# Kernel optimization log

Hardware: AMD Instinct MI355X
Metric: run time of the kernel (lower is better)

## Reference

```python
import jax, jax.numpy as jnp
import numpy as np

N_NODES, N_EDGES = 50000, 800000
IN_X, OUT_X = 32, 64
IN_EN, OUT_EN = 32, 64
HIDDEN = [64, 128, 32]  # build_mlp hidden sizes


def _mlp_params(key, dims):
    ps = []
    for i, (a, b) in enumerate(zip(dims[:-1], dims[1:])):
        k1, k2, key = jax.random.split(key, 3)
        s = 1.0 / np.sqrt(a)
        ps.append(jax.random.uniform(k1, (a, b), jnp.float32, -s, s))
        ps.append(jax.random.uniform(k2, (b,), jnp.float32, -s, s))
    return ps


def _mlp_apply(h, params):
    n_layers = len(params) // 2
    for i in range(n_layers):
        W, b = params[2 * i], params[2 * i + 1]
        h = h @ W + b
        if i < n_layers - 1:
            h = jax.nn.relu(h)
    return h


def setup_inputs() -> dict:
    key = jax.random.key(0)
    kx, ken, ks, kd, kt, kp, k_ten, k_pen = jax.random.split(key, 8)
    inp = {
        "x": jax.random.normal(kx, (N_NODES, IN_X), jnp.float32),
        "en": jax.random.normal(ken, (N_NODES, IN_EN), jnp.float32),
        "src": jax.random.randint(ks, (N_EDGES,), 0, N_NODES),
        "dst": jax.random.randint(kd, (N_EDGES,), 0, N_NODES),
    }
    # linear layers theta/phi for x
    kt1, kt2 = jax.random.split(kt)
    kp1, kp2 = jax.random.split(kp)
    s = 1.0 / np.sqrt(IN_X)
    inp["theta_W"] = jax.random.uniform(kt1, (IN_X, OUT_X), jnp.float32, -s, s)
    inp["theta_b"] = jax.random.uniform(kt2, (OUT_X,), jnp.float32, -s, s)
    inp["phi_W"] = jax.random.uniform(kp1, (IN_X, OUT_X), jnp.float32, -s, s)
    inp["phi_b"] = jax.random.uniform(kp2, (OUT_X,), jnp.float32, -s, s)
    # MLPs theta_en / phi_en: in_en -> 64 -> 128 -> 32 -> out_en
    dims = [IN_EN] + HIDDEN + [OUT_EN]
    for name, p in zip(
        ["ten_W0", "ten_b0", "ten_W1", "ten_b1", "ten_W2", "ten_b2", "ten_W3", "ten_b3"],
        _mlp_params(k_ten, dims)):
        inp[name] = p
    for name, p in zip(
        ["pen_W0", "pen_b0", "pen_W1", "pen_b1", "pen_W2", "pen_b2", "pen_W3", "pen_b3"],
        _mlp_params(k_pen, dims)):
        inp[name] = p
    return inp


def reference(x, en, src, dst,
              theta_W, theta_b, phi_W, phi_b,
              ten_W0, ten_b0, ten_W1, ten_b1, ten_W2, ten_b2, ten_W3, ten_b3,
              pen_W0, pen_b0, pen_W1, pen_b1, pen_W2, pen_b2, pen_W3, pen_b3):
    n = x.shape[0]
    ten = [ten_W0, ten_b0, ten_W1, ten_b1, ten_W2, ten_b2, ten_W3, ten_b3]
    pen = [pen_W0, pen_b0, pen_W1, pen_b1, pen_W2, pen_b2, pen_W3, pen_b3]

    # --- message: per-edge features ---
    dx = x[dst] - x[src]                       # [E, in_x]
    edge_x = dx @ theta_W + theta_b + (x @ phi_W + phi_b)[src]   # [E, out_x]
    den = en[dst] - en[src]                    # [E, in_en]
    edge_en = _mlp_apply(den, ten) + _mlp_apply(en, pen)[src]    # [E, out_en]

    # --- aggregate: max over incoming edge_x, mean over incoming edge_en ---
    deg = jax.ops.segment_sum(jnp.ones((src.shape[0],), x.dtype), dst, num_segments=n)
    has_in = (deg > 0)[:, None]
    x_new = jax.ops.segment_max(edge_x, dst, num_segments=n)
    x_new = jnp.where(has_in, x_new, 0.0)      # DGL zero-fills empty nodes
    en_sum = jax.ops.segment_sum(edge_en, dst, num_segments=n)
    en_new = en_sum / jnp.maximum(deg, 1.0)[:, None]

    # knn_graph rebuild is a library call (excluded from the kernel target);
    # return the updated node features carried by the new graph.
    return jnp.concatenate([x_new, en_new], axis=-1)  # [N, out_x + out_en]
```

## Files before the change

### kernel.cpp

```cpp
#include <hip/hip_runtime.h>

#define N_NODES 50000
#define N_EDGES 800000

typedef __attribute__((ext_vector_type(8))) short short8v;
typedef __attribute__((ext_vector_type(4))) float f32x4;

__device__ __forceinline__ ushort bf16hi(float v) {
  return (ushort)(__float_as_uint(v) >> 16);
}

__device__ __forceinline__ void split8(const float v[8], short8v& hh, short8v& ll) {
#pragma unroll
  for (int j = 0; j < 8; ++j) {
    unsigned uv = __float_as_uint(v[j]);
    hh[j] = (short)(uv >> 16);
    float hf = __uint_as_float(uv & 0xFFFF0000u);
    ll[j] = (short)(__float_as_uint(v[j] - hf) >> 16);
  }
}

#define C1_X 196
#define C1_CNT 3125
#define C1_PACK 120

constexpr int XK_THT = 0;
constexpr int XK_PHT = 2048;
constexpr int XK_THB = 4096;
constexpr int XK_PHB = 4160;
constexpr int XK_SZ  = 4224;

__global__ void __launch_bounds__(256) combo1_kernel(
    const float* __restrict__ x,
    const float* __restrict__ thW, const float* __restrict__ thB,
    const float* __restrict__ phW, const float* __restrict__ phB,
    float* __restrict__ out, float* __restrict__ gp,
    const int* __restrict__ dst, int* __restrict__ counts,
    const float* __restrict__ tW1, const float* __restrict__ tW2,
    const float* __restrict__ tW0, const float* __restrict__ pW0,
    const float* __restrict__ pW1, const float* __restrict__ pW2,
    const float* __restrict__ pW3, ushort* __restrict__ wp) {
  const int b = blockIdx.x;
  const int tid = threadIdx.x;
  if (b < C1_X) {
    __shared__ __align__(16) float sm[XK_SZ];
    for (int t = tid; t < 2048; t += 256) {
      int j = t >> 5, k = t & 31;
      sm[XK_THT + t] = thW[k * 64 + j];
      sm[XK_PHT + t] = phW[k * 64 + j];
    }
    for (int t = tid; t < 64; t += 256) {
      sm[XK_THB + t] = thB[t];
      sm[XK_PHB + t] = phB[t];
    }
    __syncthreads();
    int n = b * 256 + tid;
    if (n >= N_NODES) return;

    float xv[32];
    {
      const float4* p = (const float4*)(x + (long)n * 32);
#pragma unroll
      for (int q = 0; q < 8; ++q) {
        float4 v = p[q];
        xv[q * 4 + 0] = v.x; xv[q * 4 + 1] = v.y;
        xv[q * 4 + 2] = v.z; xv[q * 4 + 3] = v.w;
      }
    }
    float* ao = out + (long)n * 128;
    float* go = gp + (long)n * 128;
    for (int j = 0; j < 64; ++j) {
      float dth = 0.f, dph = 0.f;
#pragma unroll
      for (int k = 0; k < 32; ++k) {
        dth += xv[k] * sm[XK_THT + j * 32 + k];
        dph += xv[k] * sm[XK_PHT + j * 32 + k];
      }
      ao[j] = sm[XK_THB + j] + dth;
      go[j] = sm[XK_PHB + j] + dph - dth;
    }
  } else if (b < C1_X + C1_CNT) {
    int e = (b - C1_X) * 256 + tid;
    if (e < N_EDGES) atomicAdd(&counts[dst[e]], 1);
  } else {
    int t = (b - C1_X - C1_CNT) * 256 + tid;
    if (t >= 30720) return;
    float v;
    int hi_off, lo_off;
    if (t < 8192) {
      int fi = t >> 9, lane = (t >> 3) & 63, j = t & 7;
      int r = fi >> 1, f = fi & 1;
      int row = r * 16 + (lane & 15);
      int sig = 32 * f + 16 * (j >> 2) + 4 * ((lane >> 4) & 3) + (j & 3);
      v = tW1[sig * 128 + row];
      hi_off = t; lo_off = 8192 + t;
    } else if (t < 12288) {
      int t2 = t - 8192;
      int fi = t2 >> 9, lane = (t2 >> 3) & 63, j = t2 & 7;
      int tt = fi >> 2, f2 = fi & 3;
      int cc = tt * 16 + (lane & 15);
      int qq = (lane >> 4) & 3;
      int k2 = f2 * 32 + (j >> 2) * 16 + qq * 4 + (j & 3);
      v = tW2[k2 * 32 + cc];
      hi_off = 16384 + t2; lo_off = 20480 + t2;
    } else if (t < 14336) {
      int t3 = t - 12288;
      int fi = t3 >> 9, lane = (t3 >> 3) & 63, j = t3 & 7;
      int row = fi * 16 + (lane & 15);
      int k = (lane >> 4) * 8 + j;
      v = tW0[k * 64 + row];
      hi_off = 24576 + t3; lo_off = 26624 + t3;
    } else if (t < 16384) {
      int t4 = t - 14336;
      int fi = t4 >> 9, lane = (t4 >> 3) & 63, j = t4 & 7;
      int row = fi * 16 + (lane & 15);
      int k = (lane >> 4) * 8 + j;
      v = pW0[k * 64 + row];
      hi_off = 28672 + t4; lo_off = 30720 + t4;
    } else if (t < 24576) {
      int t5 = t - 16384;
      int fi = t5 >> 9, lane = (t5 >> 3) & 63, j = t5 & 7;
      int r = fi >> 1, f = fi & 1;
      int row = r * 16 + (lane & 15);
      int sig = 32 * f + 16 * (j >> 2) + 4 * ((lane >> 4) & 3) + (j & 3);
      v = pW1[sig * 128 + row];
      hi_off = 32768 + t5; lo_off = 40960 + t5;
    } else if (t < 28672) {
      int t6 = t - 24576;
      int fi = t6 >> 9, lane = (t6 >> 3) & 63, j = t6 & 7;
      int tt = fi >> 2, f2 = fi & 3;
      int cc = tt * 16 + (lane & 15);
      int qq = (lane >> 4) & 3;
      int k2 = f2 * 32 + (j >> 2) * 16 + qq * 4 + (j & 3);
      v = pW2[k2 * 32 + cc];
      hi_off = 49152 + t6; lo_off = 53248 + t6;
    } else {
      int t7 = t - 28672;
      int fi = t7 >> 9, lane = (t7 >> 3) & 63, j = t7 & 7;
      int row = fi * 16 + (lane & 15);
      int sig = 16 * (j >> 2) + 4 * ((lane >> 4) & 3) + (j & 3);
      v = pW3[sig * 64 + row];
      hi_off = 57344 + t7; lo_off = 59392 + t7;
    }
    ushort h = bf16hi(v);
    float hf = __uint_as_float((unsigned)h << 16);
    ushort l = bf16hi(v - hf);
    wp[hi_off] = h;
    wp[lo_off] = l;
  }
}

#define SCAN_NB ((N_NODES + 1023) / 1024)

__global__ void __launch_bounds__(1024) scan1_kernel(
    const int* __restrict__ counts, int* __restrict__ offsets,
    int* __restrict__ bsum) {
  __shared__ int wsum[16];
  int t = threadIdx.x, b = blockIdx.x;
  int idx = b * 1024 + t;
  int c = (idx < N_NODES) ? counts[idx] : 0;
  int lane = t & 63, w = t >> 6;
  int v = c;
#pragma unroll
  for (int off = 1; off < 64; off <<= 1) {
    int tt = __shfl_up(v, off);
    if (lane >= off) v += tt;
  }
  if (lane == 63) wsum[w] = v;
  __syncthreads();
  int wpre = 0;
#pragma unroll
  for (int i = 0; i < 16; ++i) {
    int tt = wsum[i];
    if (i < w) wpre += tt;
  }
  int incl = v + wpre;
  if (idx < N_NODES) offsets[idx] = incl - c;
  if (t == 1023) bsum[b] = incl;
}

__global__ void __launch_bounds__(1024) scan2_kernel(
    const int* __restrict__ bsum, int* __restrict__ offsets,
    int* __restrict__ counts) {
  __shared__ int sb[SCAN_NB];
  int t = threadIdx.x, b = blockIdx.x;
  if (t < SCAN_NB) sb[t] = bsum[t];
  __syncthreads();
  int bpre = 0;
#pragma unroll
  for (int i = 0; i < SCAN_NB; ++i) {
    int tt = sb[i];
    if (i < b) bpre += tt;
  }
  int idx = b * 1024 + t;
  if (idx < N_NODES) {
    int v = offsets[idx] + bpre;
    offsets[idx] = v;
    counts[idx] = v;
  }
  if (b == 0 && t == 0) offsets[N_NODES] = N_EDGES;
}

#define C2_EN 391
#define C2_SC 1563

__global__ void __launch_bounds__(512) combo2_kernel(
    const float* __restrict__ en, const ushort* __restrict__ wp,
    const float* __restrict__ pb0, const float* __restrict__ pb1,
    const float* __restrict__ pb2, const float* __restrict__ pb3,
    float* __restrict__ gp,
    const int* __restrict__ src, const int* __restrict__ dst,
    int* __restrict__ cursor, int2* __restrict__ csr) {
  const int b = blockIdx.x;
  const int tid = threadIdx.x;
  if (b < C2_EN) {
    __shared__ __align__(16) ushort lds[32768];
    {
      const uint4* s4 = (const uint4*)(wp + 28672);
      uint4* d4 = (uint4*)lds;
      for (int i = tid; i < 4096; i += 512) d4[i] = s4[i];
    }
    __syncthreads();
    const int lane = tid & 63, q = lane >> 4, c = lane & 15, wv = tid >> 6;
    const int n = (b * 8 + wv) * 16 + c;
    const bool valid = n < N_NODES;

    float env[8];
#pragma unroll
    for (int j = 0; j < 8; ++j) env[j] = 0.f;
    if (valid) {
      const float4* p = (const float4*)(en + (long)n * 32 + q * 8);
      float4 e0 = p[0], e1 = p[1];
      env[0] = e0.x; env[1] = e0.y; env[2] = e0.z; env[3] = e0.w;
      env[4] = e1.x; env[5] = e1.y; env[6] = e1.z; env[7] = e1.w;
    }
    short8v beh, bel;
    split8(env, beh, bel);

    const short8v* PW0H = (const short8v*)(lds);
    const short8v* PW0L = (const short8v*)(lds + 2048);
    const short8v* NW1H = (const short8v*)(lds + 4096);
    const short8v* NW1L = (const short8v*)(lds + 12288);
    const short8v* NW2H = (const short8v*)(lds + 20480);
    const short8v* NW2L = (const short8v*)(lds + 24576);
    const short8v* NW3H = (const short8v*)(lds + 28672);
    const short8v* NW3L = (const short8v*)(lds + 30720);

    float h0v[4][4];
#pragma unroll
    for (int t = 0; t < 4; ++t) {
      f32x4 a = *(const f32x4*)(pb0 + t * 16 + q * 4);
      short8v ah = PW0H[t * 64 + lane], al = PW0L[t * 64 + lane];
      a = __builtin_amdgcn_mfma_f32_16x16x32_bf16(ah, beh, a, 0, 0, 0);
      a = __builtin_amdgcn_mfma_f32_16x16x32_bf16(al, beh, a, 0, 0, 0);
      a = __builtin_amdgcn_mfma_f32_16x16x32_bf16(ah, bel, a, 0, 0, 0);
#pragma unroll
      for (int g = 0; g < 4; ++g) h0v[t][g] = fmaxf(a[g], 0.f);
    }

    short8v b1h[2], b1l[2];
#pragma unroll
    for (int f = 0; f < 2; ++f) {
      float tmp[8];
#pragma unroll
      for (int j = 0; j < 8; ++j) tmp[j] = h0v[2 * f + (j >> 2)][j & 3];
      split8(tmp, b1h[f], b1l[f]);
    }

    float h1v[8][4];
#pragma unroll
    for (int r = 0; r < 8; ++r) {
      f32x4 a = *(const f32x4*)(pb1 + r * 16 + q * 4);
#pragma unroll
      for (int f = 0; f < 2; ++f) {
        short8v ah = NW1H[(r * 2 + f) * 64 + lane];
        short8v al = NW1L[(r * 2 + f) * 64 + lane];
        a = __builtin_amdgcn_mfma_f32_16x16x32_bf16(ah, b1h[f], a, 0, 0, 0);
        a = __builtin_amdgcn_mfma_f32_16x16x32_bf16(al, b1h[f], a, 0, 0, 0);
        a = __builtin_amdgcn_mfma_f32_16x16x32_bf16(ah, b1l[f], a, 0, 0, 0);
      }
#pragma unroll
      for (int g = 0; g < 4; ++g) h1v[r][g] = fmaxf(a[g], 0.f);
    }

    short8v b2h[4], b2l[4];
#pragma unroll
    for (int f2 = 0; f2 < 4; ++f2) {
      float tmp[8];
#pragma unroll
      for (int j = 0; j < 8; ++j) tmp[j] = h1v[2 * f2 + (j >> 2)][j & 3];
      split8(tmp, b2h[f2], b2l[f2]);
    }

    float h2v[2][4];
#pragma unroll
    for (int tt = 0; tt < 2; ++tt) {
      f32x4 a = *(const f32x4*)(pb2 + tt * 16 + q * 4);
#pragma unroll
      for (int f2 = 0; f2 < 4; ++f2) {
        short8v ah = NW2H[(tt * 4 + f2) * 64 + lane];
        short8v al = NW2L[(tt * 4 + f2) * 64 + lane];
        a = __builtin_amdgcn_mfma_f32_16x16x32_bf16(ah, b2h[f2], a, 0, 0, 0);
        a = __builtin_amdgcn_mfma_f32_16x16x32_bf16(al, b2h[f2], a, 0, 0, 0);
        a = __builtin_amdgcn_mfma_f32_16x16x32_bf16(ah, b2l[f2], a, 0, 0, 0);
      }
#pragma unroll
      for (int g = 0; g < 4; ++g) h2v[tt][g] = fmaxf(a[g], 0.f);
    }

    short8v b3h, b3l;
    {
      float tmp[8];
#pragma unroll
      for (int j = 0; j < 8; ++j) tmp[j] = h2v[j >> 2][j & 3];
      split8(tmp, b3h, b3l);
    }

#pragma unroll
    for (int t = 0; t < 4; ++t) {
      f32x4 a = *(const f32x4*)(pb3 + t * 16 + q * 4);
      short8v ah = NW3H[t * 64 + lane], al = NW3L[t * 64 + lane];
      a = __builtin_amdgcn_mfma_f32_16x16x32_bf16(ah, b3h, a, 0, 0, 0);
      a = __builtin_amdgcn_mfma_f32_16x16x32_bf16(al, b3h, a, 0, 0, 0);
      a = __builtin_amdgcn_mfma_f32_16x16x32_bf16(ah, b3l, a, 0, 0, 0);
      if (valid) *(f32x4*)(gp + (long)n * 128 + 64 + t * 16 + q * 4) = a;
    }
  } else {
    int e = (b - C2_EN) * 512 + tid;
    if (e >= N_EDGES) return;
    int d = dst[e];
    int slot = atomicAdd(&cursor[d], 1);
    csr[slot] = make_int2(src[e], d);
  }
}

__global__ void __launch_bounds__(1024) mlp_edge_kernel(
    const float* __restrict__ en,
    const int2* __restrict__ csr,
    const float* __restrict__ b0g, const float* __restrict__ b1g,
    const float* __restrict__ b2g,
    const ushort* __restrict__ wp,
    float* __restrict__ h2sum) {
  __shared__ __align__(16) ushort lds[28672];
  {
    const uint4* s4 = (const uint4*)wp;
    uint4* d4 = (uint4*)lds;
    for (int i = threadIdx.x; i < 3584; i += 1024) d4[i] = s4[i];
  }
  __syncthreads();

  const int orig = blockIdx.x;
  const int xcd = orig & 7, loc = orig >> 3;
  const int blk = (xcd < 5) ? xcd * 391 + loc
                            : 5 * 391 + (xcd - 5) * 390 + loc;

  const int lane = threadIdx.x & 63;
  const int q = lane >> 4, c = lane & 15;
  const int wv = threadIdx.x >> 6;
  const int e = (blk * 16 + wv) * 16 + c;
  const int2 pr = csr[e];
  const int s = pr.x, d = pr.y;

  const short8v* W1HI = (const short8v*)(lds);
  const short8v* W1LO = (const short8v*)(lds + 8192);
  const short8v* W2HI = (const short8v*)(lds + 16384);
  const short8v* W2LO = (const short8v*)(lds + 20480);
  const short8v* W0H  = (const short8v*)(lds + 24576);
  const short8v* W0L  = (const short8v*)(lds + 26624);

  short8v dh, dl;
  {
    const float4* pd = (const float4*)(en + (long)d * 32 + q * 8);
    const float4* ps = (const float4*)(en + (long)s * 32 + q * 8);
    float4 a0 = pd[0], a1 = pd[1], b0 = ps[0], b1 = ps[1];
    float v[8];
    v[0] = a0.x - b0.x; v[1] = a0.y - b0.y;
    v[2] = a0.z - b0.z; v[3] = a0.w - b0.w;
    v[4] = a1.x - b1.x; v[5] = a1.y - b1.y;
    v[6] = a1.z - b1.z; v[7] = a1.w - b1.w;
    split8(v, dh, dl);
  }

  float h0v[4][4];
#pragma unroll
  for (int t = 0; t < 4; ++t) {
    f32x4 a = *(const f32x4*)(b0g + t * 16 + q * 4);
    short8v ah = W0H[t * 64 + lane], al = W0L[t * 64 + lane];
    a = __builtin_amdgcn_mfma_f32_16x16x32_bf16(ah, dh, a, 0, 0, 0);
    a = __builtin_amdgcn_mfma_f32_16x16x32_bf16(al, dh, a, 0, 0, 0);
    a = __builtin_amdgcn_mfma_f32_16x16x32_bf16(ah, dl, a, 0, 0, 0);
#pragma unroll
    for (int g = 0; g < 4; ++g) h0v[t][g] = fmaxf(a[g], 0.f);
  }

  short8v b1h[2], b1l[2];
#pragma unroll
  for (int f = 0; f < 2; ++f) {
    float tmp[8];
#pragma unroll
    for (int j = 0; j < 8; ++j) tmp[j] = h0v[2 * f + (j >> 2)][j & 3];
    split8(tmp, b1h[f], b1l[f]);
  }

  float h1v[8][4];
#pragma unroll
  for (int r = 0; r < 8; ++r) {
    f32x4 a = *(const f32x4*)(b1g + r * 16 + q * 4);
#pragma unroll
    for (int f = 0; f < 2; ++f) {
      short8v ah = W1HI[(r * 2 + f) * 64 + lane];
      short8v al = W1LO[(r * 2 + f) * 64 + lane];
      a = __builtin_amdgcn_mfma_f32_16x16x32_bf16(ah, b1h[f], a, 0, 0, 0);
      a = __builtin_amdgcn_mfma_f32_16x16x32_bf16(al, b1h[f], a, 0, 0, 0);
      a = __builtin_amdgcn_mfma_f32_16x16x32_bf16(ah, b1l[f], a, 0, 0, 0);
    }
#pragma unroll
    for (int g = 0; g < 4; ++g) h1v[r][g] = fmaxf(a[g], 0.f);
  }

  short8v b2h[4], b2l[4];
#pragma unroll
  for (int f2 = 0; f2 < 4; ++f2) {
    float tmp[8];
#pragma unroll
    for (int j = 0; j < 8; ++j) tmp[j] = h1v[2 * f2 + (j >> 2)][j & 3];
    split8(tmp, b2h[f2], b2l[f2]);
  }

  f32x4 a20 = *(const f32x4*)(b2g + q * 4);
  f32x4 a21 = *(const f32x4*)(b2g + 16 + q * 4);
#pragma unroll
  for (int f2 = 0; f2 < 4; ++f2) {
    short8v ah = W2HI[f2 * 64 + lane];
    short8v al = W2LO[f2 * 64 + lane];
    a20 = __builtin_amdgcn_mfma_f32_16x16x32_bf16(ah, b2h[f2], a20, 0, 0, 0);
    a20 = __builtin_amdgcn_mfma_f32_16x16x32_bf16(al, b2h[f2], a20, 0, 0, 0);
    a20 = __builtin_amdgcn_mfma_f32_16x16x32_bf16(ah, b2l[f2], a20, 0, 0, 0);
    short8v ah1 = W2HI[(4 + f2) * 64 + lane];
    short8v al1 = W2LO[(4 + f2) * 64 + lane];
    a21 = __builtin_amdgcn_mfma_f32_16x16x32_bf16(ah1, b2h[f2], a21, 0, 0, 0);
    a21 = __builtin_amdgcn_mfma_f32_16x16x32_bf16(al1, b2h[f2], a21, 0, 0, 0);
    a21 = __builtin_amdgcn_mfma_f32_16x16x32_bf16(ah1, b2l[f2], a21, 0, 0, 0);
  }
  float h2v[8];
#pragma unroll
  for (int g = 0; g < 4; ++g) {
    h2v[g] = fmaxf(a20[g], 0.f);
    h2v[4 + g] = fmaxf(a21[g], 0.f);
  }

  int dp = __shfl_up(d, 1, 16);
  bool head = (c == 0) || (dp != d);
  int seg = head ? c : 0;
#pragma unroll
  for (int off = 1; off < 16; off <<= 1) {
    int t = __shfl_up(seg, off, 16);
    if (c >= off) seg = max(seg, t);
  }
#pragma unroll
  for (int off = 1; off < 16; off <<= 1) {
    bool take = (c - off) >= seg;
#pragma unroll
    for (int k = 0; k < 8; ++k) {
      float t = __shfl_up(h2v[k], off, 16);
      if (take) h2v[k] += t;
    }
  }
  int dn = __shfl_down(d, 1, 16);
  bool tail = (c == 15) || (dn != d);
  if (tail) {
    float* hs = h2sum + (long)d * 32 + q * 4;
#pragma unroll
    for (int g = 0; g < 4; ++g) atomicAdd(&hs[g], h2v[g]);
#pragma unroll
    for (int g = 0; g < 4; ++g) atomicAdd(&hs[16 + g], h2v[4 + g]);
  }
}

__global__ void __launch_bounds__(256) gather_kernel(
    const int2* __restrict__ csr, const int* __restrict__ offsets,
    const float* __restrict__ gp, const float* __restrict__ h2sum,
    const float* __restrict__ tW3, const float* __restrict__ tb3,
    float* __restrict__ out) {
  __shared__ float sW3[2048 + 64];
  for (int t = threadIdx.x; t < 2048; t += 256) sW3[t] = tW3[t];
  for (int t = threadIdx.x; t < 64; t += 256) sW3[2048 + t] = tb3[t];
  __syncthreads();
  int n = blockIdx.x * 8 + (threadIdx.x >> 5);
  int l = threadIdx.x & 31;
  int half = l >> 4, j4 = l & 15;
  int off = half * 64 + j4 * 4;
  int o0 = offsets[n], o1 = offsets[n + 1];
  int deg = o1 - o0;

  const float NEG = -3.402823466e38f;
  float4 mx = make_float4(NEG, NEG, NEG, NEG);
  float4 sm4 = make_float4(0.f, 0.f, 0.f, 0.f);
  for (int t = o0; t < o1; ++t) {
    int s = csr[t].x;
    float4 v = *(const float4*)(gp + (long)s * 128 + off);
    mx.x = fmaxf(mx.x, v.x); mx.y = fmaxf(mx.y, v.y);
    mx.z = fmaxf(mx.z, v.z); mx.w = fmaxf(mx.w, v.w);
    sm4.x += v.x; sm4.y += v.y; sm4.z += v.z; sm4.w += v.w;
  }

  float4 r;
  if (half == 0) {
    float4 a = *(const float4*)(out + (long)n * 128 + off);
    bool has = deg > 0;
    r.x = has ? a.x + mx.x : 0.f;
    r.y = has ? a.y + mx.y : 0.f;
    r.z = has ? a.z + mx.z : 0.f;
    r.w = has ? a.w + mx.w : 0.f;
  } else {
    int jj = j4 * 4;
    float w30 = 0.f, w31 = 0.f, w32 = 0.f, w33 = 0.f;
    const float* h2r = h2sum + (long)n * 32;
#pragma unroll
    for (int k = 0; k < 32; ++k) {
      float h = h2r[k];
      const float* wrow = &sW3[k * 64 + jj];
      w30 += h * wrow[0]; w31 += h * wrow[1];
      w32 += h * wrow[2]; w33 += h * wrow[3];
    }
    float dg = (float)deg;
    float inv = 1.f / fmaxf(dg, 1.f);
    r.x = (sm4.x + w30 + dg * sW3[2048 + jj + 0]) * inv;
    r.y = (sm4.y + w31 + dg * sW3[2048 + jj + 1]) * inv;
    r.z = (sm4.z + w32 + dg * sW3[2048 + jj + 2]) * inv;
    r.w = (sm4.w + w33 + dg * sW3[2048 + jj + 3]) * inv;
  }
  *(float4*)(out + (long)n * 128 + off) = r;
}

extern "C" void kernel_launch(void* const* d_in, const int* in_sizes, int n_in,
                              void* d_out, int out_size, void* d_ws,
                              size_t ws_size, hipStream_t stream) {
  const float* x   = (const float*)d_in[0];
  const float* en  = (const float*)d_in[1];
  const int* src   = (const int*)d_in[2];
  const int* dst   = (const int*)d_in[3];
  const float* thW = (const float*)d_in[4];
  const float* thB = (const float*)d_in[5];
  const float* phW = (const float*)d_in[6];
  const float* phB = (const float*)d_in[7];
  const float* tW0 = (const float*)d_in[8];
  const float* tb0 = (const float*)d_in[9];
  const float* tW1 = (const float*)d_in[10];
  const float* tb1 = (const float*)d_in[11];
  const float* tW2 = (const float*)d_in[12];
  const float* tb2 = (const float*)d_in[13];
  const float* tW3 = (const float*)d_in[14];
  const float* tb3 = (const float*)d_in[15];
  const float* pW0 = (const float*)d_in[16];
  const float* pb0 = (const float*)d_in[17];
  const float* pW1 = (const float*)d_in[18];
  const float* pb1 = (const float*)d_in[19];
  const float* pW2 = (const float*)d_in[20];
  const float* pb2 = (const float*)d_in[21];
  const float* pW3 = (const float*)d_in[22];
  const float* pb3 = (const float*)d_in[23];

  float* out = (float*)d_out;
  float* ws  = (float*)d_ws;
  float* gp     = ws;
  float* h2sum  = ws + (long)N_NODES * 128;
  float* wpf    = ws + (long)N_NODES * 160;
  ushort* wp    = (ushort*)wpf;
  int* iw       = (int*)(wpf + 30720);
  int2* csr     = (int2*)iw;
  int* counts   = iw + 2 * N_EDGES;
  int* offsets  = counts + N_NODES;
  int* bsum     = offsets + N_NODES + 1;

  hipMemsetAsync(counts, 0, N_NODES * sizeof(int), stream);
  hipMemsetAsync(h2sum, 0, (size_t)N_NODES * 32 * sizeof(float), stream);
  combo1_kernel<<<C1_X + C1_CNT + C1_PACK, 256, 0, stream>>>(
      x, thW, thB, phW, phB, out, gp, dst, counts,
      tW1, tW2, tW0, pW0, pW1, pW2, pW3, wp);
  scan1_kernel<<<SCAN_NB, 1024, 0, stream>>>(counts, offsets, bsum);
  scan2_kernel<<<SCAN_NB, 1024, 0, stream>>>(bsum, offsets, counts);
  combo2_kernel<<<C2_EN + C2_SC, 512, 0, stream>>>(
      en, wp, pb0, pb1, pb2, pb3, gp, src, dst, counts, csr);
  mlp_edge_kernel<<<3125, 1024, 0, stream>>>(
      en, csr, tb0, tb1, tb2, wp, h2sum);
  gather_kernel<<<N_NODES / 8, 256, 0, stream>>>(
      csr, offsets, gp, h2sum, tW3, tb3, out);
}
```

Baseline: 315.2 us.

## Fuse node gather into edge MLP kernel and split out a light finalize pass

```diff
diff --git a/kernel.cpp b/kernel.cpp
--- a/kernel.cpp
+++ b/kernel.cpp
@@ -334,23 +334,64 @@
   }
 }
 
-__global__ void __launch_bounds__(1024) mlp_edge_kernel(
+#define EG_NB 4689
+
+__global__ void __launch_bounds__(1024) edge_gather_kernel(
     const float* __restrict__ en,
     const int2* __restrict__ csr,
     const float* __restrict__ b0g, const float* __restrict__ b1g,
     const float* __restrict__ b2g,
     const ushort* __restrict__ wp,
-    float* __restrict__ h2sum) {
+    float* __restrict__ h2sum,
+    const int* __restrict__ offsets,
+    const float* __restrict__ gp, float* __restrict__ out) {
   __shared__ __align__(16) ushort lds[28672];
+  const int bm = blockIdx.x % 3;
+  if (bm == 2) {
+    int gb = blockIdx.x / 3;
+    int n = gb * 32 + (threadIdx.x >> 5);
+    if (n >= N_NODES) return;
+    int l = threadIdx.x & 31;
+    int half = l >> 4, j4 = l & 15;
+    int off = half * 64 + j4 * 4;
+    int o0 = offsets[n], o1 = offsets[n + 1];
+    int deg = o1 - o0;
+
+    const float NEG = -3.402823466e38f;
+    float4 mx = make_float4(NEG, NEG, NEG, NEG);
+    float4 sm4 = make_float4(0.f, 0.f, 0.f, 0.f);
+    for (int t = o0; t < o1; ++t) {
+      int s = csr[t].x;
+      float4 v = *(const float4*)(gp + (long)s * 128 + off);
+      mx.x = fmaxf(mx.x, v.x); mx.y = fmaxf(mx.y, v.y);
+      mx.z = fmaxf(mx.z, v.z); mx.w = fmaxf(mx.w, v.w);
+      sm4.x += v.x; sm4.y += v.y; sm4.z += v.z; sm4.w += v.w;
+    }
+    float4 r;
+    if (half == 0) {
+      float4 a = *(const float4*)(out + (long)n * 128 + off);
+      bool has = deg > 0;
+      r.x = has ? a.x + mx.x : 0.f;
+      r.y = has ? a.y + mx.y : 0.f;
+      r.z = has ? a.z + mx.z : 0.f;
+      r.w = has ? a.w + mx.w : 0.f;
+    } else {
+      r = sm4;
+    }
+    *(float4*)(out + (long)n * 128 + off) = r;
+    return;
+  }
+
+  const int eb = (blockIdx.x / 3) * 2 + bm;
   {
     const uint4* s4 = (const uint4*)wp;
     uint4* d4 = (uint4*)lds;
     for (int i = threadIdx.x; i < 3584; i += 1024) d4[i] = s4[i];
   }
   __syncthreads();
-
-  const int orig = blockIdx.x;
-  const int xcd = orig & 7, loc = orig >> 3;
+  if (eb >= 3125) return;
+
+  const int xcd = eb & 7, loc = eb >> 3;
   const int blk = (xcd < 5) ? xcd * 391 + loc
                             : 5 * 391 + (xcd - 5) * 390 + loc;
 
@@ -477,60 +518,39 @@
   }
 }
 
-__global__ void __launch_bounds__(256) gather_kernel(
-    const int2* __restrict__ csr, const int* __restrict__ offsets,
-    const float* __restrict__ gp, const float* __restrict__ h2sum,
+__global__ void __launch_bounds__(256) finalize_kernel(
+    const int* __restrict__ offsets, const float* __restrict__ h2sum,
     const float* __restrict__ tW3, const float* __restrict__ tb3,
     float* __restrict__ out) {
   __shared__ float sW3[2048 + 64];
   for (int t = threadIdx.x; t < 2048; t += 256) sW3[t] = tW3[t];
   for (int t = threadIdx.x; t < 64; t += 256) sW3[2048 + t] = tb3[t];
   __syncthreads();
-  int n = blockIdx.x * 8 + (threadIdx.x >> 5);
-  int l = threadIdx.x & 31;
-  int half = l >> 4, j4 = l & 15;
-  int off = half * 64 + j4 * 4;
-  int o0 = offsets[n], o1 = offsets[n + 1];
-  int deg = o1 - o0;
-
-  const float NEG = -3.402823466e38f;
-  float4 mx = make_float4(NEG, NEG, NEG, NEG);
-  float4 sm4 = make_float4(0.f, 0.f, 0.f, 0.f);
-  for (int t = o0; t < o1; ++t) {
-    int s = csr[t].x;
-    float4 v = *(const float4*)(gp + (long)s * 128 + off);
-    mx.x = fmaxf(mx.x, v.x); mx.y = fmaxf(mx.y, v.y);
-    mx.z = fmaxf(mx.z, v.z); mx.w = fmaxf(mx.w, v.w);
-    sm4.x += v.x; sm4.y += v.y; sm4.z += v.z; sm4.w += v.w;
-  }
-
+  int n = blockIdx.x * 16 + (threadIdx.x >> 4);
+  int j4 = threadIdx.x & 15;
+  int jj = j4 * 4;
+  int deg = offsets[n + 1] - offsets[n];
+
+  float* po = out + (long)n * 128 + 64 + jj;
+  float4 ssum = *(const float4*)po;
+
+  float w30 = 0.f, w31 = 0.f, w32 = 0.f, w33 = 0.f;
+  const float* h2r = h2sum + (long)n * 32;
+#pragma unroll
+  for (int k = 0; k < 32; ++k) {
+    float h = h2r[k];
+    const float* wrow = &sW3[k * 64 + jj];
+    w30 += h * wrow[0]; w31 += h * wrow[1];
+    w32 += h * wrow[2]; w33 += h * wrow[3];
+  }
+  float dg = (float)deg;
+  float inv = 1.f / fmaxf(dg, 1.f);
   float4 r;
-  if (half == 0) {
-    float4 a = *(const float4*)(out + (long)n * 128 + off);
-    bool has = deg > 0;
-    r.x = has ? a.x + mx.x : 0.f;
-    r.y = has ? a.y + mx.y : 0.f;
-    r.z = has ? a.z + mx.z : 0.f;
-    r.w = has ? a.w + mx.w : 0.f;
-  } else {
-    int jj = j4 * 4;
-    float w30 = 0.f, w31 = 0.f, w32 = 0.f, w33 = 0.f;
-    const float* h2r = h2sum + (long)n * 32;
-#pragma unroll
-    for (int k = 0; k < 32; ++k) {
-      float h = h2r[k];
-      const float* wrow = &sW3[k * 64 + jj];
-      w30 += h * wrow[0]; w31 += h * wrow[1];
-      w32 += h * wrow[2]; w33 += h * wrow[3];
-    }
-    float dg = (float)deg;
-    float inv = 1.f / fmaxf(dg, 1.f);
-    r.x = (sm4.x + w30 + dg * sW3[2048 + jj + 0]) * inv;
-    r.y = (sm4.y + w31 + dg * sW3[2048 + jj + 1]) * inv;
-    r.z = (sm4.z + w32 + dg * sW3[2048 + jj + 2]) * inv;
-    r.w = (sm4.w + w33 + dg * sW3[2048 + jj + 3]) * inv;
-  }
-  *(float4*)(out + (long)n * 128 + off) = r;
+  r.x = (ssum.x + w30 + dg * sW3[2048 + jj + 0]) * inv;
+  r.y = (ssum.y + w31 + dg * sW3[2048 + jj + 1]) * inv;
+  r.z = (ssum.z + w32 + dg * sW3[2048 + jj + 2]) * inv;
+  r.w = (ssum.w + w33 + dg * sW3[2048 + jj + 3]) * inv;
+  *(float4*)po = r;
 }
 
 extern "C" void kernel_launch(void* const* d_in, const int* in_sizes, int n_in,
@@ -582,8 +602,8 @@
   scan2_kernel<<<SCAN_NB, 1024, 0, stream>>>(bsum, offsets, counts);
   combo2_kernel<<<C2_EN + C2_SC, 512, 0, stream>>>(
       en, wp, pb0, pb1, pb2, pb3, gp, src, dst, counts, csr);
-  mlp_edge_kernel<<<3125, 1024, 0, stream>>>(
-      en, csr, tb0, tb1, tb2, wp, h2sum);
-  gather_kernel<<<N_NODES / 8, 256, 0, stream>>>(
-      csr, offsets, gp, h2sum, tW3, tb3, out);
-}
+  edge_gather_kernel<<<EG_NB, 1024, 0, stream>>>(
+      en, csr, tb0, tb1, tb2, wp, h2sum, offsets, gp, out);
+  finalize_kernel<<<N_NODES / 16, 256, 0, stream>>>(
+      offsets, h2sum, tW3, tb3, out);
+}
```

After: 349.8 us. +11.0%, slower.

## Switch edge MLP from 16x16x32 to 32x32x16 MFMA tiles

Applied to the files above, without the earlier changes.

```diff
diff --git a/kernel.cpp b/kernel.cpp
--- a/kernel.cpp
+++ b/kernel.cpp
@@ -5,6 +5,7 @@
 
 typedef __attribute__((ext_vector_type(8))) short short8v;
 typedef __attribute__((ext_vector_type(4))) float f32x4;
+typedef __attribute__((ext_vector_type(16))) float f32x16;
 
 __device__ __forceinline__ ushort bf16hi(float v) {
   return (ushort)(__float_as_uint(v) >> 16);
@@ -89,26 +90,28 @@
     int hi_off, lo_off;
     if (t < 8192) {
       int fi = t >> 9, lane = (t >> 3) & 63, j = t & 7;
-      int r = fi >> 1, f = fi & 1;
-      int row = r * 16 + (lane & 15);
-      int sig = 32 * f + 16 * (j >> 2) + 4 * ((lane >> 4) & 3) + (j & 3);
-      v = tW1[sig * 128 + row];
+      int r = fi >> 2, kt1 = fi & 3;
+      int row = r * 32 + (lane & 31);
+      int h = (lane >> 5) & 1;
+      int k = (kt1 >> 1) * 32 + (kt1 & 1) * 16 + (j & 3) + 4 * h + 8 * (j >> 2);
+      v = tW1[k * 128 + row];
       hi_off = t; lo_off = 8192 + t;
     } else if (t < 12288) {
       int t2 = t - 8192;
-      int fi = t2 >> 9, lane = (t2 >> 3) & 63, j = t2 & 7;
-      int tt = fi >> 2, f2 = fi & 3;
-      int cc = tt * 16 + (lane & 15);
-      int qq = (lane >> 4) & 3;
-      int k2 = f2 * 32 + (j >> 2) * 16 + qq * 4 + (j & 3);
-      v = tW2[k2 * 32 + cc];
+      int kt2 = t2 >> 9, lane = (t2 >> 3) & 63, j = t2 & 7;
+      int outc = lane & 31;
+      int h = (lane >> 5) & 1;
+      int k = (kt2 >> 1) * 32 + (kt2 & 1) * 16 + (j & 3) + 4 * h + 8 * (j >> 2);
+      v = tW2[k * 32 + outc];
       hi_off = 16384 + t2; lo_off = 20480 + t2;
     } else if (t < 14336) {
       int t3 = t - 12288;
       int fi = t3 >> 9, lane = (t3 >> 3) & 63, j = t3 & 7;
-      int row = fi * 16 + (lane & 15);
-      int k = (lane >> 4) * 8 + j;
-      v = tW0[k * 64 + row];
+      int r = fi >> 1, kt = fi & 1;
+      int outc = r * 32 + (lane & 31);
+      int h = (lane >> 5) & 1;
+      int k = kt * 16 + 8 * h + j;
+      v = tW0[k * 64 + outc];
       hi_off = 24576 + t3; lo_off = 26624 + t3;
     } else if (t < 16384) {
       int t4 = t - 14336;
@@ -334,7 +337,7 @@
   }
 }
 
-__global__ void __launch_bounds__(1024) mlp_edge_kernel(
+__global__ void __launch_bounds__(512) mlp_edge_kernel(
     const float* __restrict__ en,
     const int2* __restrict__ csr,
     const float* __restrict__ b0g, const float* __restrict__ b1g,
@@ -345,7 +348,7 @@
   {
     const uint4* s4 = (const uint4*)wp;
     uint4* d4 = (uint4*)lds;
-    for (int i = threadIdx.x; i < 3584; i += 1024) d4[i] = s4[i];
+    for (int i = threadIdx.x; i < 3584; i += 512) d4[i] = s4[i];
   }
   __syncthreads();
 
@@ -355,9 +358,9 @@
                             : 5 * 391 + (xcd - 5) * 390 + loc;
 
   const int lane = threadIdx.x & 63;
-  const int q = lane >> 4, c = lane & 15;
+  const int c = lane & 31, h = lane >> 5;
   const int wv = threadIdx.x >> 6;
-  const int e = (blk * 16 + wv) * 16 + c;
+  const int e = blk * 256 + wv * 32 + c;
   const int2 pr = csr[e];
   const int s = pr.x, d = pr.y;
 
@@ -368,112 +371,120 @@
   const short8v* W0H  = (const short8v*)(lds + 24576);
   const short8v* W0L  = (const short8v*)(lds + 26624);
 
-  short8v dh, dl;
+  short8v dh0, dl0, dh1, dl1;
   {
-    const float4* pd = (const float4*)(en + (long)d * 32 + q * 8);
-    const float4* ps = (const float4*)(en + (long)s * 32 + q * 8);
-    float4 a0 = pd[0], a1 = pd[1], b0 = ps[0], b1 = ps[1];
-    float v[8];
-    v[0] = a0.x - b0.x; v[1] = a0.y - b0.y;
-    v[2] = a0.z - b0.z; v[3] = a0.w - b0.w;
-    v[4] = a1.x - b1.x; v[5] = a1.y - b1.y;
-    v[6] = a1.z - b1.z; v[7] = a1.w - b1.w;
-    split8(v, dh, dl);
-  }
-
-  float h0v[4][4];
-#pragma unroll
-  for (int t = 0; t < 4; ++t) {
-    f32x4 a = *(const f32x4*)(b0g + t * 16 + q * 4);
-    short8v ah = W0H[t * 64 + lane], al = W0L[t * 64 + lane];
-    a = __builtin_amdgcn_mfma_f32_16x16x32_bf16(ah, dh, a, 0, 0, 0);
-    a = __builtin_amdgcn_mfma_f32_16x16x32_bf16(al, dh, a, 0, 0, 0);
-    a = __builtin_amdgcn_mfma_f32_16x16x32_bf16(ah, dl, a, 0, 0, 0);
-#pragma unroll
-    for (int g = 0; g < 4; ++g) h0v[t][g] = fmaxf(a[g], 0.f);
-  }
-
-  short8v b1h[2], b1l[2];
-#pragma unroll
-  for (int f = 0; f < 2; ++f) {
+    const float4* pd = (const float4*)(en + (long)d * 32);
+    const float4* ps = (const float4*)(en + (long)s * 32);
+    float4 a0 = pd[2 * h], a1 = pd[2 * h + 1];
+    float4 s0 = ps[2 * h], s1 = ps[2 * h + 1];
+    float va[8];
+    va[0] = a0.x - s0.x; va[1] = a0.y - s0.y;
+    va[2] = a0.z - s0.z; va[3] = a0.w - s0.w;
+    va[4] = a1.x - s1.x; va[5] = a1.y - s1.y;
+    va[6] = a1.z - s1.z; va[7] = a1.w - s1.w;
+    split8(va, dh0, dl0);
+    float4 a2 = pd[4 + 2 * h], a3 = pd[5 + 2 * h];
+    float4 s2 = ps[4 + 2 * h], s3 = ps[5 + 2 * h];
+    float vb[8];
+    vb[0] = a2.x - s2.x; vb[1] = a2.y - s2.y;
+    vb[2] = a2.z - s2.z; vb[3] = a2.w - s2.w;
+    vb[4] = a3.x - s3.x; vb[5] = a3.y - s3.y;
+    vb[6] = a3.z - s3.z; vb[7] = a3.w - s3.w;
+    split8(vb, dh1, dl1);
+  }
+
+  float h0v[2][16];
+#pragma unroll
+  for (int t = 0; t < 2; ++t) {
+    f32x16 a;
+#pragma unroll
+    for (int g = 0; g < 16; ++g)
+      a[g] = b0g[t * 32 + (g & 3) + 8 * (g >> 2) + 4 * h];
+    short8v ah0 = W0H[(t * 2 + 0) * 64 + lane], al0 = W0L[(t * 2 + 0) * 64 + lane];
+    short8v ah1 = W0H[(t * 2 + 1) * 64 + lane], al1 = W0L[(t * 2 + 1) * 64 + lane];
+    a = __builtin_amdgcn_mfma_f32_32x32x16_bf16(ah0, dh0, a, 0, 0, 0);
+    a = __builtin_amdgcn_mfma_f32_32x32x16_bf16(al0, dh0, a, 0, 0, 0);
+    a = __builtin_amdgcn_mfma_f32_32x32x16_bf16(ah0, dl0, a, 0, 0, 0);
+    a = __builtin_amdgcn_mfma_f32_32x32x16_bf16(ah1, dh1, a, 0, 0, 0);
+    a = __builtin_amdgcn_mfma_f32_32x32x16_bf16(al1, dh1, a, 0, 0, 0);
+    a = __builtin_amdgcn_mfma_f32_32x32x16_bf16(ah1, dl1, a, 0, 0, 0);
+#pragma unroll
+    for (int g = 0; g < 16; ++g) h0v[t][g] = fmaxf(a[g], 0.f);
+  }
+
+  short8v b1h[4], b1l[4];
+#pragma unroll
+  for (int kt = 0; kt < 4; ++kt) {
     float tmp[8];
 #pragma unroll
-    for (int j = 0; j < 8; ++j) tmp[j] = h0v[2 * f + (j >> 2)][j & 3];
-    split8(tmp, b1h[f], b1l[f]);
-  }
-
-  float h1v[8][4];
-#pragma unroll
-  for (int r = 0; r < 8; ++r) {
-    f32x4 a = *(const f32x4*)(b1g + r * 16 + q * 4);
-#pragma unroll
-    for (int f = 0; f < 2; ++f) {
-      short8v ah = W1HI[(r * 2 + f) * 64 + lane];
-      short8v al = W1LO[(r * 2 + f) * 64 + lane];
-      a = __builtin_amdgcn_mfma_f32_16x16x32_bf16(ah, b1h[f], a, 0, 0, 0);
-      a = __builtin_amdgcn_mfma_f32_16x16x32_bf16(al, b1h[f], a, 0, 0, 0);
-      a = __builtin_amdgcn_mfma_f32_16x16x32_bf16(ah, b1l[f], a, 0, 0, 0);
-    }
-#pragma unroll
-    for (int g = 0; g < 4; ++g) h1v[r][g] = fmaxf(a[g], 0.f);
-  }
-
-  short8v b2h[4], b2l[4];
-#pragma unroll
-  for (int f2 = 0; f2 < 4; ++f2) {
+    for (int j = 0; j < 8; ++j) tmp[j] = h0v[kt >> 1][8 * (kt & 1) + j];
+    split8(tmp, b1h[kt], b1l[kt]);
+  }
+
+  float h1v[4][16];
+#pragma unroll
+  for (int r = 0; r < 4; ++r) {
+    f32x16 a;
+#pragma unroll
+    for (int g = 0; g < 16; ++g)
+      a[g] = b1g[r * 32 + (g & 3) + 8 * (g >> 2) + 4 * h];
+#pragma unroll
+    for (int kt = 0; kt < 4; ++kt) {
+      short8v ah = W1HI[(r * 4 + kt) * 64 + lane];
+      short8v al = W1LO[(r * 4 + kt) * 64 + lane];
+      a = __builtin_amdgcn_mfma_f32_32x32x16_bf16(ah, b1h[kt], a, 0, 0, 0);
+      a = __builtin_amdgcn_mfma_f32_32x32x16_bf16(al, b1h[kt], a, 0, 0, 0);
+      a = __builtin_amdgcn_mfma_f32_32x32x16_bf16(ah, b1l[kt], a, 0, 0, 0);
+    }
+#pragma unroll
+    for (int g = 0; g < 16; ++g) h1v[r][g] = fmaxf(a[g], 0.f);
+  }
+
+  f32x16 a2;
+#pragma unroll
+  for (int g = 0; g < 16; ++g)
+    a2[g] = b2g[(g & 3) + 8 * (g >> 2) + 4 * h];
+#pragma unroll
+  for (int kt2 = 0; kt2 < 8; ++kt2) {
     float tmp[8];
 #pragma unroll
-    for (int j = 0; j < 8; ++j) tmp[j] = h1v[2 * f2 + (j >> 2)][j & 3];
-    split8(tmp, b2h[f2], b2l[f2]);
-  }
-
-  f32x4 a20 = *(const f32x4*)(b2g + q * 4);
-  f32x4 a21 = *(const f32x4*)(b2g + 16 + q * 4);
-#pragma unroll
-  for (int f2 = 0; f2 < 4; ++f2) {
-    short8v ah = W2HI[f2 * 64 + lane];
-    short8v al = W2LO[f2 * 64 + lane];
-    a20 = __builtin_amdgcn_mfma_f32_16x16x32_bf16(ah, b2h[f2], a20, 0, 0, 0);
-    a20 = __builtin_amdgcn_mfma_f32_16x16x32_bf16(al, b2h[f2], a20, 0, 0, 0);
-    a20 = __builtin_amdgcn_mfma_f32_16x16x32_bf16(ah, b2l[f2], a20, 0, 0, 0);
-    short8v ah1 = W2HI[(4 + f2) * 64 + lane];
-    short8v al1 = W2LO[(4 + f2) * 64 + lane];
-    a21 = __builtin_amdgcn_mfma_f32_16x16x32_bf16(ah1, b2h[f2], a21, 0, 0, 0);
-    a21 = __builtin_amdgcn_mfma_f32_16x16x32_bf16(al1, b2h[f2], a21, 0, 0, 0);
-    a21 = __builtin_amdgcn_mfma_f32_16x16x32_bf16(ah1, b2l[f2], a21, 0, 0, 0);
-  }
-  float h2v[8];
-#pragma unroll
-  for (int g = 0; g < 4; ++g) {
-    h2v[g] = fmaxf(a20[g], 0.f);
-    h2v[4 + g] = fmaxf(a21[g], 0.f);
-  }
-
-  int dp = __shfl_up(d, 1, 16);
+    for (int j = 0; j < 8; ++j) tmp[j] = h1v[kt2 >> 1][8 * (kt2 & 1) + j];
+    short8v bh, bl;
+    split8(tmp, bh, bl);
+    short8v ah = W2HI[kt2 * 64 + lane];
+    short8v al = W2LO[kt2 * 64 + lane];
+    a2 = __builtin_amdgcn_mfma_f32_32x32x16_bf16(ah, bh, a2, 0, 0, 0);
+    a2 = __builtin_amdgcn_mfma_f32_32x32x16_bf16(al, bh, a2, 0, 0, 0);
+    a2 = __builtin_amdgcn_mfma_f32_32x32x16_bf16(ah, bl, a2, 0, 0, 0);
+  }
+  float h2v[16];
+#pragma unroll
+  for (int g = 0; g < 16; ++g) h2v[g] = fmaxf(a2[g], 0.f);
+
+  int dp = __shfl_up(d, 1, 32);
   bool head = (c == 0) || (dp != d);
   int seg = head ? c : 0;
 #pragma unroll
-  for (int off = 1; off < 16; off <<= 1) {
-    int t = __shfl_up(seg, off, 16);
+  for (int off = 1; off < 32; off <<= 1) {
+    int t = __shfl_up(seg, off, 32);
     if (c >= off) seg = max(seg, t);
   }
 #pragma unroll
-  for (int off = 1; off < 16; off <<= 1) {
+  for (int off = 1; off < 32; off <<= 1) {
     bool take = (c - off) >= seg;
 #pragma unroll
-    for (int k = 0; k < 8; ++k) {
-      float t = __shfl_up(h2v[k], off, 16);
-      if (take) h2v[k] += t;
-    }
-  }
-  int dn = __shfl_down(d, 1, 16);
-  bool tail = (c == 15) || (dn != d);
+    for (int g = 0; g < 16; ++g) {
+      float t = __shfl_up(h2v[g], off, 32);
+      if (take) h2v[g] += t;
+    }
+  }
+  int dn = __shfl_down(d, 1, 32);
+  bool tail = (c == 31) || (dn != d);
   if (tail) {
-    float* hs = h2sum + (long)d * 32 + q * 4;
-#pragma unroll
-    for (int g = 0; g < 4; ++g) atomicAdd(&hs[g], h2v[g]);
-#pragma unroll
-    for (int g = 0; g < 4; ++g) atomicAdd(&hs[16 + g], h2v[4 + g]);
+    float* hs = h2sum + (long)d * 32;
+#pragma unroll
+    for (int g = 0; g < 16; ++g)
+      atomicAdd(&hs[(g & 3) + 8 * (g >> 2) + 4 * h], h2v[g]);
   }
 }
 
@@ -582,7 +593,7 @@
   scan2_kernel<<<SCAN_NB, 1024, 0, stream>>>(bsum, offsets, counts);
   combo2_kernel<<<C2_EN + C2_SC, 512, 0, stream>>>(
       en, wp, pb0, pb1, pb2, pb3, gp, src, dst, counts, csr);
-  mlp_edge_kernel<<<3125, 1024, 0, stream>>>(
+  mlp_edge_kernel<<<3125, 512, 0, stream>>>(
       en, csr, tb0, tb1, tb2, wp, h2sum);
   gather_kernel<<<N_NODES / 8, 256, 0, stream>>>(
       csr, offsets, gp, h2sum, tW3, tb3, out);
```

Result: slower. 335.0 us (+6.3%).
